# Performance work log

Hardware: AMD Instinct MI355X
Metric: run time of the kernel (lower is better)

## Reference

```python
import jax, jax.numpy as jnp
import numpy as np

N_ATOMS = 500000
N_EDGES = 16000000
MAX_Z = 94


def setup_inputs() -> dict:
    key = jax.random.key(0)
    k1, k2, k3, k4 = jax.random.split(key, 4)
    Z = jax.random.randint(k1, (N_ATOMS,), 0, MAX_Z, dtype=jnp.int32)
    # distances in a physically plausible short range (ZBL is a short-range repulsion)
    Dij = jax.random.uniform(k2, (N_EDGES,), dtype=jnp.float32)
    idx_i = jnp.sort(jax.random.randint(k3, (N_EDGES,), 0, N_ATOMS, dtype=jnp.int32))
    idx_j = jax.random.randint(k4, (N_EDGES,), 0, N_ATOMS, dtype=jnp.int32)
    # learned parameters (defaults from ZBL.__init__)
    p = jnp.float32(0.23)
    d = jnp.float32(0.885)
    c = jnp.array([0.1818, 0.5099, 0.2802, 0.02817], dtype=jnp.float32)
    a = jnp.array([3.2, 0.9423, 0.4028, 0.2016], dtype=jnp.float32)
    return {"Z": Z, "Dij": Dij, "idx_i": idx_i, "idx_j": idx_j,
            "p": p, "d": d, "c": c, "a": a}


def reference(Z, Dij, idx_i, idx_j, p, d, c, a):
    # gather per-edge atomic numbers
    Zi = Z[idx_i].astype(Dij.dtype)  # [E]
    Zj = Z[idx_j].astype(Dij.dtype)  # [E]
    # NOTE: the original computes pre = Zi*Zj/Dij but never uses it in vij;
    # we reproduce the math actually returned.
    expv = Dij / d * (Zi ** p + Zj ** p)  # [E]
    # sum over the 4 screening terms: c[k] * exp(-a[k] * expv)
    vij = jnp.einsum("k,ke->e", c, jnp.exp(-a[:, None] * expv[None, :]))  # [E]
    # per-atom reduction (tf.math.segment_sum with sorted idx_i)
    return jax.ops.segment_sum(vij, idx_i, num_segments=N_ATOMS)  # [N]
```

## Files before the change

kernel.cpp:

```cpp
#include <hip/hip_runtime.h>


#define EPT   16
#define BLOCK 256
#define MAXZ  95

__device__ __forceinline__ float fast_exp2(float x) {
#if __has_builtin(__builtin_amdgcn_exp2f)
    return __builtin_amdgcn_exp2f(x);
#else
    return exp2f(x);
#endif
}

__global__ void __launch_bounds__(BLOCK) zbl_stage_kernel(
    const int* __restrict__ Z, const float* __restrict__ p,
    unsigned char* __restrict__ z8, float* __restrict__ zpf,
    float* __restrict__ ptab, int n)
{
    int i = blockIdx.x * BLOCK + threadIdx.x;
    if (i < MAXZ) ptab[i] = powf((float)i, p[0]);
    if (i < n) {
        int z = Z[i];
        z8[i]  = (unsigned char)z;
        zpf[i] = powf((float)z, p[0]);
    }
}

__global__ void __launch_bounds__(BLOCK) zbl_edge_kernel(
    const float*         __restrict__ Dij,
    const int*           __restrict__ idx_i,
    const int*           __restrict__ idx_j,
    const unsigned char* __restrict__ z8,
    const float*         __restrict__ zpf,
    const float*         __restrict__ ptab_g,
    const float*         __restrict__ dptr,
    const float*         __restrict__ c,
    const float*         __restrict__ a,
    float*               __restrict__ out,
    long long E)
{
    __shared__ float pt[MAXZ + 1];
    for (int k = threadIdx.x; k < MAXZ; k += BLOCK) pt[k] = ptab_g[k];
    __syncthreads();

    const long long t    = (long long)blockIdx.x * BLOCK + threadIdx.x;
    const long long base = t * EPT;
    if (base >= E) return;

    const float LOG2E = 1.4426950408889634f;
    const float invd  = 1.0f / dptr[0];
    const float m0 = -a[0] * LOG2E * invd;
    const float m1 = -a[1] * LOG2E * invd;
    const float m2 = -a[2] * LOG2E * invd;
    const float m3 = -a[3] * LOG2E * invd;
    const float c0 = c[0], c1 = c[1], c2 = c[2], c3 = c[3];

    if (base + EPT <= E) {
        float dv[EPT];
        int   iv[EPT], jv[EPT];
#pragma unroll
        for (int v = 0; v < EPT; v += 4) {
            const float4 dq = *reinterpret_cast<const float4*>(Dij  + base + v);
            const int4   iq = *reinterpret_cast<const int4*>(idx_i + base + v);
            const int4   jq = *reinterpret_cast<const int4*>(idx_j + base + v);
            dv[v] = dq.x; dv[v+1] = dq.y; dv[v+2] = dq.z; dv[v+3] = dq.w;
            iv[v] = iq.x; iv[v+1] = iq.y; iv[v+2] = iq.z; iv[v+3] = iq.w;
            jv[v] = jq.x; jv[v+1] = jq.y; jv[v+2] = jq.z; jv[v+3] = jq.w;
        }
        float zpj[EPT];
#pragma unroll
        for (int k = 0; k < EPT; ++k) {
            zpj[k] = __hip_atomic_load(zpf + jv[k], __ATOMIC_RELAXED,
                                       __HIP_MEMORY_SCOPE_AGENT);
        }
        int zi[EPT];
#pragma unroll
        for (int k = 0; k < EPT; ++k) zi[k] = z8[iv[k]];

        int   cur = iv[0];
        float acc = 0.0f;
#pragma unroll
        for (int k = 0; k < EPT; ++k) {
            const float tt = dv[k] * (pt[zi[k]] + zpj[k]);
            float v;
            v = c0 * fast_exp2(m0 * tt);
            v = fmaf(c1, fast_exp2(m1 * tt), v);
            v = fmaf(c2, fast_exp2(m2 * tt), v);
            v = fmaf(c3, fast_exp2(m3 * tt), v);
            if (iv[k] != cur) { atomicAdd(out + cur, acc); acc = 0.0f; cur = iv[k]; }
            acc += v;
        }
        atomicAdd(out + cur, acc);
    } else {
        int   cur = idx_i[base];
        float acc = 0.0f;
        for (long long e = base; e < E; ++e) {
            const int   i  = idx_i[e];
            const float zj = __hip_atomic_load(zpf + idx_j[e], __ATOMIC_RELAXED,
                                               __HIP_MEMORY_SCOPE_AGENT);
            const float tt = Dij[e] * (pt[z8[i]] + zj);
            float v;
            v = c0 * fast_exp2(m0 * tt);
            v = fmaf(c1, fast_exp2(m1 * tt), v);
            v = fmaf(c2, fast_exp2(m2 * tt), v);
            v = fmaf(c3, fast_exp2(m3 * tt), v);
            if (i != cur) { atomicAdd(out + cur, acc); acc = 0.0f; cur = i; }
            acc += v;
        }
        atomicAdd(out + cur, acc);
    }
}

extern "C" void kernel_launch(void* const* d_in, const int* in_sizes, int n_in,
                              void* d_out, int out_size, void* d_ws, size_t ws_size,
                              hipStream_t stream)
{
    const int*   Z     = (const int*)  d_in[0];
    const float* Dij   = (const float*)d_in[1];
    const int*   idx_i = (const int*)  d_in[2];
    const int*   idx_j = (const int*)  d_in[3];
    const float* p     = (const float*)d_in[4];
    const float* d     = (const float*)d_in[5];
    const float* c     = (const float*)d_in[6];
    const float* a     = (const float*)d_in[7];
    float*       out   = (float*)d_out;

    const int       nAtoms = in_sizes[0];
    const long long E      = in_sizes[1];

    float*         zpf  = (float*)d_ws;
    unsigned char* z8   = (unsigned char*)d_ws + (size_t)nAtoms * sizeof(float);
    size_t         poff = ((size_t)nAtoms * sizeof(float) + (size_t)nAtoms + 63) & ~(size_t)63;
    float*         ptab = (float*)((char*)d_ws + poff);

    (void)hipMemsetAsync(d_out, 0, (size_t)out_size * sizeof(float), stream);

    zbl_stage_kernel<<<(nAtoms + BLOCK - 1) / BLOCK, BLOCK, 0, stream>>>(
        Z, p, z8, zpf, ptab, nAtoms);

    const long long nThreads = (E + EPT - 1) / EPT;
    const int       nBlocks  = (int)((nThreads + BLOCK - 1) / BLOCK);
    zbl_edge_kernel<<<nBlocks, BLOCK, 0, stream>>>(
        Dij, idx_i, idx_j, z8, zpf, ptab, d, c, a, out, E);
}
```

Before: 257.3 us.

## Stage first 128K atom Z bytes in LDS and reuse per-run i lookups

Each 1024-thread block copies the first 131072 bytes of the per-atom Z table plus the power table into LDS. Random idx_j lookups that fall in that range are served from LDS instead of global memory. The idx_i side reads the precomputed power directly and reuses it across the sorted run (first/last atom). The cost is a 128KB LDS copy per block across roughly 1000 blocks, which is about 128MB of extra reads. It also sharply limits occupancy, since one 1024-thread block per CU uses most of the 160KB LDS.

Result: slower. 287.7 us (+11.8%).

```diff
diff --git a/kernel.cpp b/kernel.cpp
--- a/kernel.cpp
+++ b/kernel.cpp
@@ -1,9 +1,10 @@
 #include <hip/hip_runtime.h>
 
 
-#define EPT   16
-#define BLOCK 256
-#define MAXZ  95
+#define EPT    16
+#define BLOCK  1024
+#define MAXZ   96
+#define SL     131072
 
 __device__ __forceinline__ float fast_exp2(float x) {
 #if __has_builtin(__builtin_amdgcn_exp2f)
@@ -13,12 +14,12 @@
 #endif
 }
 
-__global__ void __launch_bounds__(BLOCK) zbl_stage_kernel(
+__global__ void __launch_bounds__(256) zbl_stage_kernel(
     const int* __restrict__ Z, const float* __restrict__ p,
     unsigned char* __restrict__ z8, float* __restrict__ zpf,
     float* __restrict__ ptab, int n)
 {
-    int i = blockIdx.x * BLOCK + threadIdx.x;
+    int i = blockIdx.x * 256 + threadIdx.x;
     if (i < MAXZ) ptab[i] = powf((float)i, p[0]);
     if (i < n) {
         int z = Z[i];
@@ -40,8 +41,16 @@
     float*               __restrict__ out,
     long long E)
 {
-    __shared__ float pt[MAXZ + 1];
-    for (int k = threadIdx.x; k < MAXZ; k += BLOCK) pt[k] = ptab_g[k];
+    extern __shared__ char smem[];
+    unsigned char* s_z8 = (unsigned char*)smem;
+    float*         s_pt = (float*)(smem + SL);
+
+    for (int k = threadIdx.x; k < MAXZ; k += BLOCK) s_pt[k] = ptab_g[k];
+    {
+        const uint4* src = (const uint4*)z8;
+        uint4*       dst = (uint4*)s_z8;
+        for (int k = threadIdx.x; k < SL / 16; k += BLOCK) dst[k] = src[k];
+    }
     __syncthreads();
 
     const long long t    = (long long)blockIdx.x * BLOCK + threadIdx.x;
@@ -71,18 +80,29 @@
         float zpj[EPT];
 #pragma unroll
         for (int k = 0; k < EPT; ++k) {
-            zpj[k] = __hip_atomic_load(zpf + jv[k], __ATOMIC_RELAXED,
-                                       __HIP_MEMORY_SCOPE_AGENT);
+            const int j = jv[k];
+            if (j < SL) {
+                zpj[k] = s_pt[s_z8[j]];
+            } else {
+                zpj[k] = __hip_atomic_load(zpf + j, __ATOMIC_RELAXED,
+                                           __HIP_MEMORY_SCOPE_AGENT);
+            }
         }
-        int zi[EPT];
+        const int   iFirst  = iv[0], iLast = iv[EPT - 1];
+        const float zpFirst = zpf[iFirst];
+        const float zpLast  = (iLast == iFirst) ? zpFirst : zpf[iLast];
+        float zpi[EPT];
 #pragma unroll
-        for (int k = 0; k < EPT; ++k) zi[k] = z8[iv[k]];
-
-        int   cur = iv[0];
+        for (int k = 0; k < EPT; ++k) {
+            zpi[k] = (iv[k] == iFirst) ? zpFirst
+                   : (iv[k] == iLast)  ? zpLast
+                   : zpf[iv[k]];
+        }
+        int   cur = iFirst;
         float acc = 0.0f;
 #pragma unroll
         for (int k = 0; k < EPT; ++k) {
-            const float tt = dv[k] * (pt[zi[k]] + zpj[k]);
+            const float tt = dv[k] * (zpi[k] + zpj[k]);
             float v;
             v = c0 * fast_exp2(m0 * tt);
             v = fmaf(c1, fast_exp2(m1 * tt), v);
@@ -97,9 +117,11 @@
         float acc = 0.0f;
         for (long long e = base; e < E; ++e) {
             const int   i  = idx_i[e];
-            const float zj = __hip_atomic_load(zpf + idx_j[e], __ATOMIC_RELAXED,
-                                               __HIP_MEMORY_SCOPE_AGENT);
-            const float tt = Dij[e] * (pt[z8[i]] + zj);
+            const int   j  = idx_j[e];
+            const float zj = (j < SL) ? s_pt[s_z8[j]]
+                                      : __hip_atomic_load(zpf + j, __ATOMIC_RELAXED,
+                                                          __HIP_MEMORY_SCOPE_AGENT);
+            const float tt = Dij[e] * (zpf[i] + zj);
             float v;
             v = c0 * fast_exp2(m0 * tt);
             v = fmaf(c1, fast_exp2(m1 * tt), v);
@@ -129,18 +151,23 @@
     const int       nAtoms = in_sizes[0];
     const long long E      = in_sizes[1];
 
-    float*         zpf  = (float*)d_ws;
-    unsigned char* z8   = (unsigned char*)d_ws + (size_t)nAtoms * sizeof(float);
-    size_t         poff = ((size_t)nAtoms * sizeof(float) + (size_t)nAtoms + 63) & ~(size_t)63;
-    float*         ptab = (float*)((char*)d_ws + poff);
+    float*         zpf   = (float*)d_ws;
+    size_t         zoff  = ((size_t)nAtoms * sizeof(float) + 15) & ~(size_t)15;
+    unsigned char* z8    = (unsigned char*)d_ws + zoff;
+    size_t         poff  = (zoff + (size_t)nAtoms + 63) & ~(size_t)63;
+    float*         ptab  = (float*)((char*)d_ws + poff);
 
     (void)hipMemsetAsync(d_out, 0, (size_t)out_size * sizeof(float), stream);
 
-    zbl_stage_kernel<<<(nAtoms + BLOCK - 1) / BLOCK, BLOCK, 0, stream>>>(
+    zbl_stage_kernel<<<(nAtoms + 255) / 256, 256, 0, stream>>>(
         Z, p, z8, zpf, ptab, nAtoms);
+
+    const int dynLds = SL + MAXZ * (int)sizeof(float);
+    (void)hipFuncSetAttribute((const void*)zbl_edge_kernel,
+                              hipFuncAttributeMaxDynamicSharedMemorySize, dynLds);
 
     const long long nThreads = (E + EPT - 1) / EPT;
     const int       nBlocks  = (int)((nThreads + BLOCK - 1) / BLOCK);
-    zbl_edge_kernel<<<nBlocks, BLOCK, 0, stream>>>(
+    zbl_edge_kernel<<<nBlocks, BLOCK, dynLds, stream>>>(
         Dij, idx_i, idx_j, z8, zpf, ptab, d, c, a, out, E);
 }
```
